# Kernel tuning notes

Hardware: AMD Instinct MI355X
Metric: run time of the kernel (lower is better)

Reference implementation:

```python
import jax, jax.numpy as jnp
import numpy as np

N_NODES = 50000
N_EDGES = 1600000
CHANNELS = 128
EXPANSION = 50
CUTOFF = 5.0
LOG2 = 0.6931471805599453


def shifted_softplus(x):
    return jax.nn.softplus(x) - LOG2


def gaussian_smearing(r, cutoff=CUTOFF, n=EXPANSION):
    # centers evenly spaced in [0, cutoff]; width set by spacing
    centers = jnp.linspace(0.0, cutoff, n, dtype=r.dtype)
    delta = centers[1] - centers[0]
    coef = 1.0 / (2.0 * delta * delta)
    d = r[:, None] - centers[None, :]          # [E, n]
    return jnp.exp(-coef * d * d)


def setup_inputs() -> dict:
    key = jax.random.key(0)
    ks = jax.random.split(key, 12)
    C, F = CHANNELS, EXPANSION

    def lin(k, fan_in, shape):
        bound = 1.0 / np.sqrt(fan_in)
        return jax.random.uniform(k, shape, jnp.float32, -bound, bound)

    return {
        "features": jax.random.normal(ks[0], (N_NODES, C), jnp.float32),
        "edge_distances": jax.random.uniform(ks[1], (N_EDGES,), jnp.float32) * CUTOFF,
        "W_lin": lin(ks[2], C, (C, C)),
        "Wf1": lin(ks[3], F, (F, C)), "bf1": lin(ks[4], F, (C,)),
        "Wf2": lin(ks[5], C, (C, C)), "bf2": lin(ks[6], C, (C,)),
        "Wm1": lin(ks[7], C, (C, C)), "bm1": lin(ks[8], C, (C,)),
        "Wm2": lin(ks[9], C, (C, C)), "bm2": lin(ks[10], C, (C,)),
        "senders": jax.random.randint(ks[11], (N_EDGES,), 0, N_NODES, jnp.int32),
        "receivers": jax.random.randint(jax.random.fold_in(key, 99), (N_EDGES,), 0, N_NODES, jnp.int32),
    }


def reference(features, edge_distances, W_lin, Wf1, bf1, Wf2, bf2,
              Wm1, bm1, Wm2, bm2, senders, receivers):
    # 1. linear transform of node features (no bias)
    h = features @ W_lin.T                                   # [N, C]
    # 2. learnable radial filter F(r_ij): Gaussian basis -> MLP
    basis = gaussian_smearing(edge_distances)                # [E, F]
    ef = shifted_softplus(basis @ Wf1 + bf1) @ Wf2 + bf2     # [E, C]
    # 3. gather neighbour features, elementwise multiply, scatter-sum
    messages = h[senders] * ef                               # [E, C]
    agg = jax.ops.segment_sum(messages, receivers, num_segments=N_NODES)  # [N, C]
    # 4. output MLP
    return shifted_softplus(agg @ Wm1 + bm1) @ Wm2 + bm2
```

## Files before the change

### kernel.cpp

```cpp
#include <hip/hip_runtime.h>
#include <hip/hip_bf16.h>
#include <math.h>

#define N_NODES 50000
#define N_EDGES 1600000
#define CH 128
#define NF 50
#define NR 8192
#define NB 512
#define BUCKET_NODES 98
#define CAP 3584
#define PASSA_CHUNK 4096
#define NBLK_SCAT 391
#define NBLK_TB   128
#define NBLK_DH   782

constexpr float DELTA  = 5.0f / 49.0f;
constexpr float COEF   = 1.0f / (2.0f * DELTA * DELTA);
constexpr float LOG2_  = 0.6931471805599453f;
constexpr float RSCALE = (float)(NR - 1) / 5.0f;

typedef short  bf16x8 __attribute__((ext_vector_type(8)));
typedef float  f32x4  __attribute__((ext_vector_type(4)));
typedef unsigned short ushort_t;
typedef unsigned long long u64;

__device__ __forceinline__ float ssp(float x) {
    return fmaxf(x, 0.0f) + __logf(1.0f + __expf(-fabsf(x))) - LOG2_;
}
__device__ __forceinline__ ushort_t f2bf(float x) {
    __hip_bfloat16 b = __float2bfloat16(x);
    return *reinterpret_cast<ushort_t*>(&b);
}
__device__ __forceinline__ float bf2f(ushort_t u) {
    return __uint_as_float(((unsigned)u) << 16);
}
__device__ __forceinline__ float4 f4zero() { return make_float4(0.f, 0.f, 0.f, 0.f); }

__global__ __launch_bounds__(256) void k1_prep(const float* __restrict__ Wlin,
                                               const float* __restrict__ Wm1,
                                               const float* __restrict__ Wm2,
                                               const float* __restrict__ Wf1,
                                               const float* __restrict__ Wf2,
                                               ushort_t* __restrict__ wlhi,
                                               ushort_t* __restrict__ wllo,
                                               ushort_t* __restrict__ wm1hi,
                                               ushort_t* __restrict__ wm1lo,
                                               ushort_t* __restrict__ wm2hi,
                                               ushort_t* __restrict__ wm2lo,
                                               ushort_t* __restrict__ wf1t,
                                               ushort_t* __restrict__ wf2hi,
                                               ushort_t* __restrict__ wf2lo,
                                               int* __restrict__ bcnt) {
    const int tid = threadIdx.x;
    if (blockIdx.x == 64) {
        bcnt[tid] = 0;
        bcnt[tid + 256] = 0;
        return;
    }
    int idx = blockIdx.x * 256 + tid;
    int n = idx >> 7, k = idx & 127;
    {   float w = Wlin[(size_t)n * CH + k];
        ushort_t hi = f2bf(w); wlhi[n * CH + k] = hi; wllo[n * CH + k] = f2bf(w - bf2f(hi)); }
    {   float w = Wm1[(size_t)k * CH + n];
        ushort_t hi = f2bf(w); wm1hi[n * CH + k] = hi; wm1lo[n * CH + k] = f2bf(w - bf2f(hi)); }
    {   float w = Wm2[(size_t)k * CH + n];
        ushort_t hi = f2bf(w); wm2hi[n * CH + k] = hi; wm2lo[n * CH + k] = f2bf(w - bf2f(hi)); }
    if (k < 64) wf1t[n * 64 + k] = (k < NF) ? f2bf(Wf1[k * CH + n]) : (ushort_t)0;
    {   float w = Wf2[(size_t)k * CH + n];
        ushort_t hi = f2bf(w); wf2hi[n * CH + k] = hi; wf2lo[n * CH + k] = f2bf(w - bf2f(hi)); }
}

__device__ void scatter_body(char* smem, int blk,
                             const int* __restrict__ recv,
                             const int* __restrict__ send,
                             const float* __restrict__ dist,
                             int* __restrict__ bcnt,
                             u64* __restrict__ brec) {
    int* bcur   = (int*)smem;
    int* bbaseL = bcur + NB;
    const int tid = threadIdx.x;
    for (int i = tid; i < NB; i += 256) bcur[i] = 0;
    __syncthreads();
    const int e0 = blk * PASSA_CHUNK;
#pragma unroll
    for (int i = 0; i < 16; i++) {
        int e = e0 + tid + i * 256;
        if (e < N_EDGES) atomicAdd(&bcur[recv[e] / BUCKET_NODES], 1);
    }
    __syncthreads();
    for (int i = tid; i < NB; i += 256) {
        int c = bcur[i];
        bbaseL[i] = c ? atomicAdd(&bcnt[i], c) : 0;
        bcur[i] = 0;
    }
    __syncthreads();
#pragma unroll
    for (int i = 0; i < 16; i++) {
        int e = e0 + tid + i * 256;
        if (e < N_EDGES) {
            int r = recv[e];
            int b = r / BUCKET_NODES;
            int rank = bbaseL[b] + atomicAdd(&bcur[b], 1);
            if (rank < CAP) {
                float x = fminf(dist[e] * RSCALE, (float)(NR - 1));
                int ti = __float2int_rn(x);
                u64 rec = (u64)(unsigned)(send[e] | (r << 16)) | ((u64)ti << 32);
                brec[(size_t)b * CAP + rank] = rec;
            }
        }
    }
}

__device__ void table_body(char* smem, int blk,
                           const float* __restrict__ bf1,
                           const float* __restrict__ bf2,
                           const ushort_t* __restrict__ wf1t,
                           const ushort_t* __restrict__ wf2hi,
                           const ushort_t* __restrict__ wf2lo,
                           ushort_t* __restrict__ tabn) {
    ushort_t (*basis)[72] = (ushort_t (*)[72])smem;
    ushort_t (*t1s)[136]  = (ushort_t (*)[136])(smem + 64 * 72 * 2);
    const int tid = threadIdx.x;
    const int g0  = blk * 64;

    for (int i = tid; i < 64 * 64; i += 256) {
        int e = i >> 6, k = i & 63;
        float val = 0.f;
        if (k < NF) {
            float r = (float)(g0 + e) * (5.0f / (float)(NR - 1));
            float d = r - (float)k * DELTA;
            val = __expf(-COEF * d * d);
        }
        basis[e][k] = f2bf(val);
    }
    __syncthreads();

    const int lane = tid & 63;
    const int wv   = tid >> 6;
    const int row  = lane & 15;
    const int quad = lane >> 4;
    const int c0   = (2 * wv) * 16 + row;
    const int c1   = c0 + 16;

    f32x4 acc[2][4];
#pragma unroll
    for (int j = 0; j < 2; j++)
#pragma unroll
        for (int rt = 0; rt < 4; rt++) acc[j][rt] = (f32x4){0.f, 0.f, 0.f, 0.f};

#pragma unroll
    for (int kb = 0; kb < 64; kb += 32) {
        bf16x8 B0 = *(const bf16x8*)&wf1t[c0 * 64 + kb + quad * 8];
        bf16x8 B1 = *(const bf16x8*)&wf1t[c1 * 64 + kb + quad * 8];
#pragma unroll
        for (int rt = 0; rt < 4; rt++) {
            bf16x8 A = *(const bf16x8*)&basis[rt * 16 + row][kb + quad * 8];
            acc[0][rt] = __builtin_amdgcn_mfma_f32_16x16x32_bf16(A, B0, acc[0][rt], 0, 0, 0);
            acc[1][rt] = __builtin_amdgcn_mfma_f32_16x16x32_bf16(A, B1, acc[1][rt], 0, 0, 0);
        }
    }
    {
        float b1v[2] = { bf1[c0], bf1[c1] };
#pragma unroll
        for (int j = 0; j < 2; j++) {
            int c = j ? c1 : c0;
#pragma unroll
            for (int rt = 0; rt < 4; rt++)
#pragma unroll
                for (int rg = 0; rg < 4; rg++) {
                    int e = rt * 16 + quad * 4 + rg;
                    t1s[e][c] = f2bf(ssp(acc[j][rt][rg] + b1v[j]));
                }
        }
    }
    __syncthreads();

#pragma unroll
    for (int j = 0; j < 2; j++)
#pragma unroll
        for (int rt = 0; rt < 4; rt++) acc[j][rt] = (f32x4){0.f, 0.f, 0.f, 0.f};

#pragma unroll
    for (int kb = 0; kb < 128; kb += 32) {
        bf16x8 B0h = *(const bf16x8*)&wf2hi[c0 * CH + kb + quad * 8];
        bf16x8 B0l = *(const bf16x8*)&wf2lo[c0 * CH + kb + quad * 8];
        bf16x8 B1h = *(const bf16x8*)&wf2hi[c1 * CH + kb + quad * 8];
        bf16x8 B1l = *(const bf16x8*)&wf2lo[c1 * CH + kb + quad * 8];
#pragma unroll
        for (int rt = 0; rt < 4; rt++) {
            bf16x8 A = *(const bf16x8*)&t1s[rt * 16 + row][kb + quad * 8];
            acc[0][rt] = __builtin_amdgcn_mfma_f32_16x16x32_bf16(A, B0l, acc[0][rt], 0, 0, 0);
            acc[0][rt] = __builtin_amdgcn_mfma_f32_16x16x32_bf16(A, B0h, acc[0][rt], 0, 0, 0);
            acc[1][rt] = __builtin_amdgcn_mfma_f32_16x16x32_bf16(A, B1l, acc[1][rt], 0, 0, 0);
            acc[1][rt] = __builtin_amdgcn_mfma_f32_16x16x32_bf16(A, B1h, acc[1][rt], 0, 0, 0);
        }
    }
    {
        float b2v[2] = { bf2[c0], bf2[c1] };
#pragma unroll
        for (int j = 0; j < 2; j++) {
            int c = j ? c1 : c0;
#pragma unroll
            for (int rt = 0; rt < 4; rt++)
#pragma unroll
                for (int rg = 0; rg < 4; rg++) {
                    int g = g0 + rt * 16 + quad * 4 + rg;
                    tabn[(size_t)g * CH + c] = f2bf(acc[j][rt][rg] + b2v[j]);
                }
        }
    }
}

__device__ void dense_h_body(char* smem, int blk,
                             const float* __restrict__ X,
                             const ushort_t* __restrict__ Bhi,
                             const ushort_t* __restrict__ Blo,
                             ushort_t* __restrict__ Y) {
    ushort_t (*xs)[136] = (ushort_t (*)[136])smem;
    const int tid  = threadIdx.x;
    const int row0 = blk * 64;

#pragma unroll
    for (int i = 0; i < 8; i++) {
        int idx = tid + i * 256;
        int r   = idx >> 5;
        int c4  = (idx & 31) * 4;
        float4 v = (row0 + r < N_NODES) ? *(const float4*)&X[(size_t)(row0 + r) * CH + c4]
                                        : f4zero();
        ushort4 s;
        s.x = f2bf(v.x); s.y = f2bf(v.y); s.z = f2bf(v.z); s.w = f2bf(v.w);
        *(ushort4*)&xs[r][c4] = s;
    }
    __syncthreads();

    const int lane = tid & 63;
    const int wv   = tid >> 6;
    const int row  = lane & 15;
    const int quad = lane >> 4;
    const int c0   = (2 * wv) * 16 + row;
    const int c1   = c0 + 16;

    f32x4 acc[2][4];
#pragma unroll
    for (int j = 0; j < 2; j++)
#pragma unroll
        for (int rt = 0; rt < 4; rt++) acc[j][rt] = (f32x4){0.f, 0.f, 0.f, 0.f};

#pragma unroll
    for (int kb = 0; kb < 128; kb += 32) {
        bf16x8 B0h = *(const bf16x8*)&Bhi[(size_t)c0 * CH + kb + quad * 8];
        bf16x8 B0l = *(const bf16x8*)&Blo[(size_t)c0 * CH + kb + quad * 8];
        bf16x8 B1h = *(const bf16x8*)&Bhi[(size_t)c1 * CH + kb + quad * 8];
        bf16x8 B1l = *(const bf16x8*)&Blo[(size_t)c1 * CH + kb + quad * 8];
#pragma unroll
        for (int rt = 0; rt < 4; rt++) {
            bf16x8 A = *(const bf16x8*)&xs[rt * 16 + row][kb + quad * 8];
            acc[0][rt] = __builtin_amdgcn_mfma_f32_16x16x32_bf16(A, B0l, acc[0][rt], 0, 0, 0);
            acc[0][rt] = __builtin_amdgcn_mfma_f32_16x16x32_bf16(A, B0h, acc[0][rt], 0, 0, 0);
            acc[1][rt] = __builtin_amdgcn_mfma_f32_16x16x32_bf16(A, B1l, acc[1][rt], 0, 0, 0);
            acc[1][rt] = __builtin_amdgcn_mfma_f32_16x16x32_bf16(A, B1h, acc[1][rt], 0, 0, 0);
        }
    }

#pragma unroll
    for (int j = 0; j < 2; j++) {
        int c = j ? c1 : c0;
#pragma unroll
        for (int rt = 0; rt < 4; rt++)
#pragma unroll
            for (int rg = 0; rg < 4; rg++) {
                int r = row0 + rt * 16 + quad * 4 + rg;
                if (r < N_NODES) Y[(size_t)r * CH + c] = f2bf(acc[j][rt][rg]);
            }
    }
}

__global__ __launch_bounds__(256) void k2_mega(const int* __restrict__ recv,
                                               const int* __restrict__ send,
                                               const float* __restrict__ dist,
                                               int* __restrict__ bcnt,
                                               u64* __restrict__ brec,
                                               const float* __restrict__ bf1,
                                               const float* __restrict__ bf2,
                                               const ushort_t* __restrict__ wf1t,
                                               const ushort_t* __restrict__ wf2hi,
                                               const ushort_t* __restrict__ wf2lo,
                                               ushort_t* __restrict__ tabn,
                                               const float* __restrict__ X,
                                               const ushort_t* __restrict__ wlhi,
                                               const ushort_t* __restrict__ wllo,
                                               ushort_t* __restrict__ h) {
    __shared__ __align__(16) char smem[64 * 72 * 2 + 64 * 136 * 2];
    const int blk = blockIdx.x;
    if (blk < NBLK_SCAT) {
        scatter_body(smem, blk, recv, send, dist, bcnt, brec);
    } else if (blk < NBLK_SCAT + NBLK_TB) {
        table_body(smem, blk - NBLK_SCAT, bf1, bf2, wf1t, wf2hi, wf2lo, tabn);
    } else {
        dense_h_body(smem, blk - NBLK_SCAT - NBLK_TB, X, wlhi, wllo, h);
    }
}

__global__ __launch_bounds__(256) void sort_gather(const int* __restrict__ bcnt,
                                                   const u64* __restrict__ brec,
                                                   const ushort_t* __restrict__ h,
                                                   const ushort_t* __restrict__ tabn,
                                                   ushort_t* __restrict__ aggb) {
    __shared__ int shist[BUCKET_NODES];
    __shared__ int sbeg[BUCKET_NODES];
    __shared__ int sexc[BUCKET_NODES];
    __shared__ unsigned sout[CAP];
    const int b = blockIdx.x, tid = threadIdx.x;
    const int nbase = b * BUCKET_NODES;
    const int nn = min(BUCKET_NODES, N_NODES - nbase);
    if (nn <= 0) return;
    const int m = min(bcnt[b], CAP);
    const u64* my = brec + (size_t)b * CAP;

    for (int i = tid; i < nn; i += 256) shist[i] = 0;
    __syncthreads();
    for (int i = tid; i < m; i += 256) {
        int l = (int)((my[i] >> 16) & 0xFFFF) - nbase;
        atomicAdd(&shist[l], 1);
    }
    __syncthreads();
    if (tid == 0) {
        int acc = 0;
        for (int l = 0; l < nn; l++) { sexc[l] = acc; acc += shist[l]; }
    }
    __syncthreads();
    for (int l = tid; l < nn; l += 256) sbeg[l] = sexc[l];
    __syncthreads();
    for (int i = tid; i < m; i += 256) {
        u64 rec = my[i];
        int l = (int)((rec >> 16) & 0xFFFF) - nbase;
        int rank = atomicAdd(&sexc[l], 1);
        sout[rank] = (unsigned)(rec & 0xFFFF) | ((unsigned)((rec >> 32) & 0x3FFF) << 16);
    }
    __syncthreads();

    const int g  = tid >> 5;
    const int c4 = (tid & 31) * 4;
    for (int l = g; l < nn; l += 8) {
        const int beg = sbeg[l], end = sbeg[l] + shist[l];
        float4 macc = f4zero();
        int e = beg;
        for (; e + 4 <= end; e += 4) {
            int s[4], ti[4];
#pragma unroll
            for (int u = 0; u < 4; u++) {
                unsigned v = sout[e + u];
                s[u]  = (int)(v & 0xFFFF);
                ti[u] = (int)(v >> 16);
            }
            ushort4 hu[4], tn[4];
#pragma unroll
            for (int u = 0; u < 4; u++) {
                hu[u] = *(const ushort4*)&h[(size_t)s[u] * CH + c4];
                tn[u] = *(const ushort4*)&tabn[(size_t)ti[u] * CH + c4];
            }
#pragma unroll
            for (int u = 0; u < 4; u++) {
                macc.x = fmaf(bf2f(hu[u].x), bf2f(tn[u].x), macc.x);
                macc.y = fmaf(bf2f(hu[u].y), bf2f(tn[u].y), macc.y);
                macc.z = fmaf(bf2f(hu[u].z), bf2f(tn[u].z), macc.z);
                macc.w = fmaf(bf2f(hu[u].w), bf2f(tn[u].w), macc.w);
            }
        }
        for (; e < end; e++) {
            unsigned v = sout[e];
            int s  = (int)(v & 0xFFFF);
            int ti = (int)(v >> 16);
            ushort4 hu = *(const ushort4*)&h[(size_t)s * CH + c4];
            ushort4 tn = *(const ushort4*)&tabn[(size_t)ti * CH + c4];
            macc.x = fmaf(bf2f(hu.x), bf2f(tn.x), macc.x);
            macc.y = fmaf(bf2f(hu.y), bf2f(tn.y), macc.y);
            macc.z = fmaf(bf2f(hu.z), bf2f(tn.z), macc.z);
            macc.w = fmaf(bf2f(hu.w), bf2f(tn.w), macc.w);
        }
        ushort4 o;
        o.x = f2bf(macc.x); o.y = f2bf(macc.y); o.z = f2bf(macc.z); o.w = f2bf(macc.w);
        *(ushort4*)&aggb[(size_t)(nbase + l) * CH + c4] = o;
    }
}

__global__ __launch_bounds__(256) void out_mlp(const ushort_t* __restrict__ AGG,
                                               const ushort_t* __restrict__ B1hi,
                                               const ushort_t* __restrict__ B1lo,
                                               const float* __restrict__ bm1,
                                               const ushort_t* __restrict__ B2hi,
                                               const ushort_t* __restrict__ B2lo,
                                               const float* __restrict__ bm2,
                                               float* __restrict__ OUT, int M) {
    __shared__ ushort_t xs[64][136];
    __shared__ ushort_t ts[64][136];
    const int tid  = threadIdx.x;
    const int row0 = blockIdx.x * 64;

#pragma unroll
    for (int i = 0; i < 4; i++) {
        int idx = tid + i * 256;
        int r   = idx >> 4;
        int c8  = (idx & 15) * 8;
        uint4 v = (row0 + r < M) ? *(const uint4*)&AGG[(size_t)(row0 + r) * CH + c8]
                                 : make_uint4(0, 0, 0, 0);
        *(uint4*)&xs[r][c8] = v;
    }
    __syncthreads();

    const int lane = tid & 63;
    const int wv   = tid >> 6;
    const int row  = lane & 15;
    const int quad = lane >> 4;
    const int c0   = (2 * wv) * 16 + row;
    const int c1   = c0 + 16;

    f32x4 acc[2][4];
#pragma unroll
    for (int j = 0; j < 2; j++)
#pragma unroll
        for (int rt = 0; rt < 4; rt++) acc[j][rt] = (f32x4){0.f, 0.f, 0.f, 0.f};

#pragma unroll
    for (int kb = 0; kb < 128; kb += 32) {
        bf16x8 B0h = *(const bf16x8*)&B1hi[(size_t)c0 * CH + kb + quad * 8];
        bf16x8 B0l = *(const bf16x8*)&B1lo[(size_t)c0 * CH + kb + quad * 8];
        bf16x8 B1h_ = *(const bf16x8*)&B1hi[(size_t)c1 * CH + kb + quad * 8];
        bf16x8 B1l_ = *(const bf16x8*)&B1lo[(size_t)c1 * CH + kb + quad * 8];
#pragma unroll
        for (int rt = 0; rt < 4; rt++) {
            bf16x8 A = *(const bf16x8*)&xs[rt * 16 + row][kb + quad * 8];
            acc[0][rt] = __builtin_amdgcn_mfma_f32_16x16x32_bf16(A, B0l, acc[0][rt], 0, 0, 0);
            acc[0][rt] = __builtin_amdgcn_mfma_f32_16x16x32_bf16(A, B0h, acc[0][rt], 0, 0, 0);
            acc[1][rt] = __builtin_amdgcn_mfma_f32_16x16x32_bf16(A, B1l_, acc[1][rt], 0, 0, 0);
            acc[1][rt] = __builtin_amdgcn_mfma_f32_16x16x32_bf16(A, B1h_, acc[1][rt], 0, 0, 0);
        }
    }
    {
        float bv[2] = { bm1[c0], bm1[c1] };
#pragma unroll
        for (int j = 0; j < 2; j++) {
            int c = j ? c1 : c0;
#pragma unroll
            for (int rt = 0; rt < 4; rt++)
#pragma unroll
                for (int rg = 0; rg < 4; rg++)
                    ts[rt * 16 + quad * 4 + rg][c] = f2bf(ssp(acc[j][rt][rg] + bv[j]));
        }
    }
    __syncthreads();

#pragma unroll
    for (int j = 0; j < 2; j++)
#pragma unroll
        for (int rt = 0; rt < 4; rt++) acc[j][rt] = (f32x4){0.f, 0.f, 0.f, 0.f};

#pragma unroll
    for (int kb = 0; kb < 128; kb += 32) {
        bf16x8 B0h = *(const bf16x8*)&B2hi[(size_t)c0 * CH + kb + quad * 8];
        bf16x8 B0l = *(const bf16x8*)&B2lo[(size_t)c0 * CH + kb + quad * 8];
        bf16x8 B1h_ = *(const bf16x8*)&B2hi[(size_t)c1 * CH + kb + quad * 8];
        bf16x8 B1l_ = *(const bf16x8*)&B2lo[(size_t)c1 * CH + kb + quad * 8];
#pragma unroll
        for (int rt = 0; rt < 4; rt++) {
            bf16x8 A = *(const bf16x8*)&ts[rt * 16 + row][kb + quad * 8];
            acc[0][rt] = __builtin_amdgcn_mfma_f32_16x16x32_bf16(A, B0l, acc[0][rt], 0, 0, 0);
            acc[0][rt] = __builtin_amdgcn_mfma_f32_16x16x32_bf16(A, B0h, acc[0][rt], 0, 0, 0);
            acc[1][rt] = __builtin_amdgcn_mfma_f32_16x16x32_bf16(A, B1l_, acc[1][rt], 0, 0, 0);
            acc[1][rt] = __builtin_amdgcn_mfma_f32_16x16x32_bf16(A, B1h_, acc[1][rt], 0, 0, 0);
        }
    }
    {
        float bv[2] = { bm2[c0], bm2[c1] };
#pragma unroll
        for (int j = 0; j < 2; j++) {
            int c = j ? c1 : c0;
#pragma unroll
            for (int rt = 0; rt < 4; rt++)
#pragma unroll
                for (int rg = 0; rg < 4; rg++) {
                    int r = row0 + rt * 16 + quad * 4 + rg;
                    if (r < M) OUT[(size_t)r * CH + c] = acc[j][rt][rg] + bv[j];
                }
        }
    }
}

extern "C" void kernel_launch(void* const* d_in, const int* in_sizes, int n_in,
                              void* d_out, int out_size, void* d_ws, size_t ws_size,
                              hipStream_t stream) {
    const float* features = (const float*)d_in[0];
    const float* dist     = (const float*)d_in[1];
    const float* W_lin    = (const float*)d_in[2];
    const float* Wf1      = (const float*)d_in[3];
    const float* bf1      = (const float*)d_in[4];
    const float* Wf2      = (const float*)d_in[5];
    const float* bf2      = (const float*)d_in[6];
    const float* Wm1      = (const float*)d_in[7];
    const float* bm1      = (const float*)d_in[8];
    const float* Wm2      = (const float*)d_in[9];
    const float* bm2      = (const float*)d_in[10];
    const int* senders    = (const int*)d_in[11];
    const int* receivers  = (const int*)d_in[12];
    float* out = (float*)d_out;

    u64* brec       = (u64*)d_ws;
    ushort_t* h     = (ushort_t*)(brec + (size_t)NB * CAP);
    ushort_t* aggb  = h + (size_t)N_NODES * CH;
    ushort_t* tabn  = aggb + (size_t)N_NODES * CH;
    int* bcnt       = (int*)(tabn + (size_t)NR * CH);
    ushort_t* wlhi  = (ushort_t*)(bcnt + NB);
    ushort_t* wllo  = wlhi  + CH * CH;
    ushort_t* wm1hi = wllo  + CH * CH;
    ushort_t* wm1lo = wm1hi + CH * CH;
    ushort_t* wm2hi = wm1lo + CH * CH;
    ushort_t* wm2lo = wm2hi + CH * CH;
    ushort_t* wf1t  = wm2lo + CH * CH;
    ushort_t* wf2hi = wf1t  + CH * 64;
    ushort_t* wf2lo = wf2hi + CH * CH;

    k1_prep<<<65, 256, 0, stream>>>(W_lin, Wm1, Wm2, Wf1, Wf2,
                                    wlhi, wllo, wm1hi, wm1lo, wm2hi, wm2lo,
                                    wf1t, wf2hi, wf2lo, bcnt);

    k2_mega<<<NBLK_SCAT + NBLK_TB + NBLK_DH, 256, 0, stream>>>(
        receivers, senders, dist, bcnt, brec,
        bf1, bf2, wf1t, wf2hi, wf2lo, tabn,
        features, wlhi, wllo, h);

    sort_gather<<<NB, 256, 0, stream>>>(bcnt, brec, h, tabn, aggb);

    out_mlp<<<NBLK_DH, 256, 0, stream>>>(aggb, wm1hi, wm1lo, bm1,
                                         wm2hi, wm2lo, bm2, out, N_NODES);
}
```

Before: 260.9 us.

## Split bucket sort from gather and run per-node gather with 16-byte loads

The fused sort+gather kernel is split in two. The first kernel sorts each bucket in shared memory and writes the sorted records, plus per-node begin offsets and counts, back to global memory. A new gather kernel with 3125 blocks handles 16 nodes per block, with 16 threads per node each loading 8 bf16 channels. This spreads the gather over far more blocks than the 512 buckets allowed and widens the loads. The cost is an extra kernel launch and a global round-trip for the sorted records, and per-node degree imbalance now falls within a block.

```diff
diff --git a/kernel.cpp b/kernel.cpp
--- a/kernel.cpp
+++ b/kernel.cpp
@@ -14,6 +14,8 @@
 #define NBLK_SCAT 391
 #define NBLK_TB   128
 #define NBLK_DH   782
+#define GATHER_NPB 16
+#define NBLK_GATH 3125
 
 constexpr float DELTA  = 5.0f / 49.0f;
 constexpr float COEF   = 1.0f / (2.0f * DELTA * DELTA);
@@ -302,13 +304,11 @@
     }
 }
 
-__global__ __launch_bounds__(256) void sort_gather(const int* __restrict__ bcnt,
-                                                   const u64* __restrict__ brec,
-                                                   const ushort_t* __restrict__ h,
-                                                   const ushort_t* __restrict__ tabn,
-                                                   ushort_t* __restrict__ aggb) {
+__global__ __launch_bounds__(256) void bucket_sort(const int* __restrict__ bcnt,
+                                                   u64* __restrict__ brec,
+                                                   int* __restrict__ nodebeg,
+                                                   int* __restrict__ nodecnt) {
     __shared__ int shist[BUCKET_NODES];
-    __shared__ int sbeg[BUCKET_NODES];
     __shared__ int sexc[BUCKET_NODES];
     __shared__ unsigned sout[CAP];
     const int b = blockIdx.x, tid = threadIdx.x;
@@ -330,7 +330,10 @@
         for (int l = 0; l < nn; l++) { sexc[l] = acc; acc += shist[l]; }
     }
     __syncthreads();
-    for (int l = tid; l < nn; l += 256) sbeg[l] = sexc[l];
+    for (int l = tid; l < nn; l += 256) {
+        nodebeg[nbase + l] = b * (CAP * 2) + sexc[l];
+        nodecnt[nbase + l] = shist[l];
+    }
     __syncthreads();
     for (int i = tid; i < m; i += 256) {
         u64 rec = my[i];
@@ -339,50 +342,61 @@
         sout[rank] = (unsigned)(rec & 0xFFFF) | ((unsigned)((rec >> 32) & 0x3FFF) << 16);
     }
     __syncthreads();
-
-    const int g  = tid >> 5;
-    const int c4 = (tid & 31) * 4;
-    for (int l = g; l < nn; l += 8) {
-        const int beg = sbeg[l], end = sbeg[l] + shist[l];
-        float4 macc = f4zero();
-        int e = beg;
-        for (; e + 4 <= end; e += 4) {
-            int s[4], ti[4];
-#pragma unroll
-            for (int u = 0; u < 4; u++) {
-                unsigned v = sout[e + u];
-                s[u]  = (int)(v & 0xFFFF);
-                ti[u] = (int)(v >> 16);
-            }
-            ushort4 hu[4], tn[4];
-#pragma unroll
-            for (int u = 0; u < 4; u++) {
-                hu[u] = *(const ushort4*)&h[(size_t)s[u] * CH + c4];
-                tn[u] = *(const ushort4*)&tabn[(size_t)ti[u] * CH + c4];
-            }
-#pragma unroll
-            for (int u = 0; u < 4; u++) {
-                macc.x = fmaf(bf2f(hu[u].x), bf2f(tn[u].x), macc.x);
-                macc.y = fmaf(bf2f(hu[u].y), bf2f(tn[u].y), macc.y);
-                macc.z = fmaf(bf2f(hu[u].z), bf2f(tn[u].z), macc.z);
-                macc.w = fmaf(bf2f(hu[u].w), bf2f(tn[u].w), macc.w);
-            }
-        }
-        for (; e < end; e++) {
-            unsigned v = sout[e];
-            int s  = (int)(v & 0xFFFF);
-            int ti = (int)(v >> 16);
-            ushort4 hu = *(const ushort4*)&h[(size_t)s * CH + c4];
-            ushort4 tn = *(const ushort4*)&tabn[(size_t)ti * CH + c4];
-            macc.x = fmaf(bf2f(hu.x), bf2f(tn.x), macc.x);
-            macc.y = fmaf(bf2f(hu.y), bf2f(tn.y), macc.y);
-            macc.z = fmaf(bf2f(hu.z), bf2f(tn.z), macc.z);
-            macc.w = fmaf(bf2f(hu.w), bf2f(tn.w), macc.w);
-        }
-        ushort4 o;
-        o.x = f2bf(macc.x); o.y = f2bf(macc.y); o.z = f2bf(macc.z); o.w = f2bf(macc.w);
-        *(ushort4*)&aggb[(size_t)(nbase + l) * CH + c4] = o;
-    }
+    unsigned* out32 = (unsigned*)(brec + (size_t)b * CAP);
+    for (int i = tid; i < m; i += 256) out32[i] = sout[i];
+}
+
+__global__ __launch_bounds__(256) void gather_nodes(const unsigned* __restrict__ recs,
+                                                    const int* __restrict__ nodebeg,
+                                                    const int* __restrict__ nodecnt,
+                                                    const ushort_t* __restrict__ h,
+                                                    const ushort_t* __restrict__ tabn,
+                                                    ushort_t* __restrict__ aggb) {
+    const int g  = threadIdx.x >> 4;
+    const int c8 = (threadIdx.x & 15) * 8;
+    const int n  = blockIdx.x * GATHER_NPB + g;
+    if (n >= N_NODES) return;
+    const int beg = nodebeg[n];
+    const int cnt = nodecnt[n];
+
+    float acc[8];
+#pragma unroll
+    for (int j = 0; j < 8; j++) acc[j] = 0.f;
+
+    int e = 0;
+    for (; e + 4 <= cnt; e += 4) {
+        unsigned v[4];
+#pragma unroll
+        for (int u = 0; u < 4; u++) v[u] = recs[beg + e + u];
+        bf16x8 hu[4], tn[4];
+#pragma unroll
+        for (int u = 0; u < 4; u++) {
+            int s  = (int)(v[u] & 0xFFFF);
+            int ti = (int)(v[u] >> 16);
+            hu[u] = *(const bf16x8*)&h[(size_t)s * CH + c8];
+            tn[u] = *(const bf16x8*)&tabn[(size_t)ti * CH + c8];
+        }
+#pragma unroll
+        for (int u = 0; u < 4; u++)
+#pragma unroll
+            for (int j = 0; j < 8; j++)
+                acc[j] = fmaf(bf2f((ushort_t)hu[u][j]), bf2f((ushort_t)tn[u][j]), acc[j]);
+    }
+    for (; e < cnt; e++) {
+        unsigned v = recs[beg + e];
+        int s  = (int)(v & 0xFFFF);
+        int ti = (int)(v >> 16);
+        bf16x8 hu = *(const bf16x8*)&h[(size_t)s * CH + c8];
+        bf16x8 tn = *(const bf16x8*)&tabn[(size_t)ti * CH + c8];
+#pragma unroll
+        for (int j = 0; j < 8; j++)
+            acc[j] = fmaf(bf2f((ushort_t)hu[j]), bf2f((ushort_t)tn[j]), acc[j]);
+    }
+
+    bf16x8 o;
+#pragma unroll
+    for (int j = 0; j < 8; j++) o[j] = (short)f2bf(acc[j]);
+    *(bf16x8*)&aggb[(size_t)n * CH + c8] = o;
 }
 
 __global__ __launch_bounds__(256) void out_mlp(const ushort_t* __restrict__ AGG,
@@ -519,6 +533,8 @@
     ushort_t* wf1t  = wm2lo + CH * CH;
     ushort_t* wf2hi = wf1t  + CH * 64;
     ushort_t* wf2lo = wf2hi + CH * CH;
+    int* nodebeg    = (int*)(wf2lo + CH * CH);
+    int* nodecnt    = nodebeg + N_NODES;
 
     k1_prep<<<65, 256, 0, stream>>>(W_lin, Wm1, Wm2, Wf1, Wf2,
                                     wlhi, wllo, wm1hi, wm1lo, wm2hi, wm2lo,
@@ -529,7 +545,10 @@
         bf1, bf2, wf1t, wf2hi, wf2lo, tabn,
         features, wlhi, wllo, h);
 
-    sort_gather<<<NB, 256, 0, stream>>>(bcnt, brec, h, tabn, aggb);
+    bucket_sort<<<NB, 256, 0, stream>>>(bcnt, brec, nodebeg, nodecnt);
+
+    gather_nodes<<<NBLK_GATH, 256, 0, stream>>>((const unsigned*)brec,
+                                                nodebeg, nodecnt, h, tabn, aggb);
 
     out_mlp<<<NBLK_DH, 256, 0, stream>>>(aggb, wm1hi, wm1lo, bm1,
                                          wm2hi, wm2lo, bm2, out, N_NODES);
```

Measured after the change: 270.5 us. 1.04x slower.
